# Optimization experiments

Hardware: AMD Instinct MI355X
Metric: run time of the kernel (lower is better)

The kernel has to match this reference:

```python
import jax, jax.numpy as jnp
import numpy as np

B, T, C = 4, 1024, 2048
H, DN, DR = 16, 128, 64
D = DN + DR  # 192
Q_RANK, KV_RANK = 1536, 512
ROPE_BASE = 10000.0


def rope_cos_sin(seq_len, dim, dtype=jnp.float32):
    inv_freq = 1.0 / (ROPE_BASE ** (jnp.arange(0, dim, 2, dtype=jnp.float32) / dim))
    t = jnp.arange(seq_len, dtype=jnp.float32)
    freqs = jnp.outer(t, inv_freq)  # [T, dim/2]
    return jnp.cos(freqs).astype(dtype), jnp.sin(freqs).astype(dtype)


def apply_rope(x, cos, sin):
    # x: [B, T, H, Dr], cos/sin: [T, Dr/2]; interleaved-pair rotation (Llama style)
    x1 = x[..., 0::2]
    x2 = x[..., 1::2]
    c = cos[None, :, None, :]
    s = sin[None, :, None, :]
    o1 = x1 * c - x2 * s
    o2 = x1 * s + x2 * c
    return jnp.stack([o1, o2], axis=-1).reshape(x.shape)


def setup_inputs() -> dict:
    key = jax.random.key(0)
    ks = jax.random.split(key, 9)
    def g(k, shape, scale):
        return jax.random.normal(k, shape, dtype=jnp.float32) * scale
    return {
        "x": g(ks[0], (B, T, C), 1.0),
        "wq_down": g(ks[1], (C, Q_RANK), C ** -0.5),
        "wq_nope": g(ks[2], (Q_RANK, H * DN), Q_RANK ** -0.5),
        "wq_rope": g(ks[3], (Q_RANK, H * DR), Q_RANK ** -0.5),
        "wkv_down": g(ks[4], (C, KV_RANK), C ** -0.5),
        "wv_up": g(ks[5], (KV_RANK, H * D), KV_RANK ** -0.5),
        "wk_nope": g(ks[6], (KV_RANK, H * DN), KV_RANK ** -0.5),
        "wk_rope": g(ks[7], (KV_RANK, H * DR), KV_RANK ** -0.5),
        "wo": g(ks[8], (H * D, C), (H * D) ** -0.5),
    }


def reference(x, wq_down, wq_nope, wq_rope, wkv_down, wv_up, wk_nope, wk_rope, wo):
    b, t, c = x.shape
    q_latent = x @ wq_down            # [B,T,Q_RANK]
    kv_latent = x @ wkv_down          # [B,T,KV_RANK]
    q_c = (q_latent @ wq_nope).reshape(b, t, H, DN)
    q_r = (q_latent @ wq_rope).reshape(b, t, H, DR)
    v = (kv_latent @ wv_up).reshape(b, t, H, D)
    k_c = (kv_latent @ wk_nope).reshape(b, t, H, DN)
    k_r = (kv_latent @ wk_rope).reshape(b, t, H, DR)

    cos, sin = rope_cos_sin(t, DR, x.dtype)
    q_r = apply_rope(q_r, cos, sin)
    k_r = apply_rope(k_r, cos, sin)

    q = jnp.concatenate([q_c, q_r], axis=-1)  # [B,T,H,D]
    k = jnp.concatenate([k_c, k_r], axis=-1)  # [B,T,H,D]

    scale = 1.0 / (D ** 0.5)
    scores = jnp.einsum("bthd,bshd->bhts", q, k) * scale  # [B,H,T,T]
    causal = jnp.tril(jnp.ones((t, t), dtype=bool))
    scores = jnp.where(causal[None, None], scores, jnp.finfo(scores.dtype).min)
    probs = jax.nn.softmax(scores, axis=-1)
    out = jnp.einsum("bhts,bshd->bthd", probs, v).reshape(b, t, H * D)
    return out @ wo
```

## Files before the change

kernel.cpp:

```cpp
#include <hip/hip_runtime.h>

typedef unsigned short u16;
typedef __bf16  bf16x8 __attribute__((ext_vector_type(8)));
typedef short   short8 __attribute__((ext_vector_type(8)));
typedef float   f32x4  __attribute__((ext_vector_type(4)));
typedef u16     u16x4  __attribute__((ext_vector_type(4)));

__device__ __forceinline__ u16 f2bf(float f) {
  unsigned b = __builtin_bit_cast(unsigned, f);
  b += 0x7fffu + ((b >> 16) & 1u);
  return (u16)(b >> 16);
}
__device__ __forceinline__ float bf2f(u16 u) {
  return __builtin_bit_cast(float, (unsigned)u << 16);
}
__device__ __forceinline__ f32x4 mfma16(short8 a, short8 b, f32x4 c) {
  return __builtin_amdgcn_mfma_f32_16x16x32_bf16(
      __builtin_bit_cast(bf16x8, a), __builtin_bit_cast(bf16x8, b), c, 0, 0, 0);
}
__device__ __forceinline__ void gload_lds16(const void* g, void* l) {
  __builtin_amdgcn_global_load_lds(
      (const __attribute__((address_space(1))) void*)g,
      (__attribute__((address_space(3))) void*)l, 16, 0, 0);
}

#define VMCNT(n) asm volatile("s_waitcnt vmcnt(" #n ")" ::: "memory")
#define MEMFENCE asm volatile("" ::: "memory")

__global__ __launch_bounds__(256) void castk(const float* __restrict__ in,
                                             u16* __restrict__ out, int n4) {
  int i = blockIdx.x * 256 + threadIdx.x;
  if (i >= n4) return;
  float4 v = ((const float4*)in)[i];
  u16x4 o;
  o[0] = f2bf(v.x); o[1] = f2bf(v.y); o[2] = f2bf(v.z); o[3] = f2bf(v.w);
  *(u16x4*)&out[i * 4] = o;
}

__global__ __launch_bounds__(256) void wcast(
    const float* __restrict__ wqd, const float* __restrict__ wqn,
    const float* __restrict__ wqr, const float* __restrict__ wkd,
    const float* __restrict__ wvu, const float* __restrict__ wkn,
    const float* __restrict__ wkr, const float* __restrict__ wo,
    u16* __restrict__ W1t, u16* __restrict__ Wqt,
    u16* __restrict__ Wkvt, u16* __restrict__ Wot) {
  __shared__ float tile[64][65];
  const int bid = blockIdx.x;
  const float* W; u16* Wt; int K, N, lid;
  if (bid < 768)       { W = wqd; Wt = W1t;                 K = 2048; N = 1536; lid = bid; }
  else if (bid < 1024) { W = wkd; Wt = W1t + 1536ull * 2048; K = 2048; N = 512;  lid = bid - 768; }
  else if (bid < 1792) { W = wqn; Wt = Wqt;                 K = 1536; N = 2048; lid = bid - 1024; }
  else if (bid < 2176) { W = wqr; Wt = Wqt + 2048ull * 1536; K = 1536; N = 1024; lid = bid - 1792; }
  else if (bid < 2432) { W = wkn; Wt = Wkvt;                K = 512;  N = 2048; lid = bid - 2176; }
  else if (bid < 2560) { W = wkr; Wt = Wkvt + 2048ull * 512; K = 512;  N = 1024; lid = bid - 2432; }
  else if (bid < 2944) { W = wvu; Wt = Wkvt + 3072ull * 512; K = 512;  N = 3072; lid = bid - 2560; }
  else                 { W = wo;  Wt = Wot;                 K = 3072; N = 2048; lid = bid - 2944; }
  const int kb = K >> 6;
  const int k0 = (lid % kb) * 64, n0 = (lid / kb) * 64;
  const int tc = threadIdx.x & 63, tr = threadIdx.x >> 6;
#pragma unroll
  for (int r = tr; r < 64; r += 4)
    tile[r][tc] = W[(size_t)(k0 + r) * N + n0 + tc];
  __syncthreads();
#pragma unroll
  for (int r = tr; r < 64; r += 4)
    Wt[(size_t)(n0 + r) * K + k0 + tc] = f2bf(tile[tc][r]);
}

template <int EPI>
__global__ __launch_bounds__(512, 2) void gemm8(const u16* __restrict__ A, int lda,
                                                const u16* __restrict__ Bt, int ldb,
                                                void* __restrict__ out0,
                                                void* __restrict__ out1,
                                                void* __restrict__ out2, int ldc,
                                                int K) {
  __shared__ char smem[98304];
  const int tid = threadIdx.x;
  const int w = tid >> 6, l = tid & 63;
  const int wr = w >> 2, wc = w & 3;
  const int lr = l & 15, lk8b = (l >> 4) << 4, lg4 = (l >> 4) * 4;

  const int nbx = gridDim.x;
  int id = blockIdx.y * nbx + blockIdx.x;
  int cpx = (nbx * gridDim.y) >> 3;
  int sid = (id & 7) * cpx + (id >> 3);
  const int m0 = (sid % nbx) * 128, n0 = (sid / nbx) * 256;

  const int arow = w * 16 + (l >> 2);
  const int acb = ((l & 3) << 4) ^ ((arow & 3) << 4);
  const u16* ag = A + (size_t)(m0 + arow) * lda + (acb >> 1);
  const int brow = w * 32 + (l >> 2);
  const int bcb = ((l & 3) << 4) ^ ((brow & 3) << 4);
  const u16* bg0 = Bt + (size_t)(n0 + brow) * ldb + (bcb >> 1);
  const u16* bg1 = bg0 + (size_t)16 * ldb;

  const int swzf = (lr & 3) << 4;
  int aoff[4], boff[4];
#pragma unroll
  for (int m = 0; m < 4; ++m)
    aoff[m] = (wr * 64 + m * 16 + lr) * 64 + (lk8b ^ swzf);
#pragma unroll
  for (int n = 0; n < 4; ++n)
    boff[n] = (wc * 64 + n * 16 + lr) * 64 + (lk8b ^ swzf);

  f32x4 acc[4][4] = {};

  auto STAGE = [&](int kt) {
    const int koff = kt << 5;
    char* ab = smem + ((kt & 3) << 13);
    char* bb = smem + 32768 + ((kt & 3) << 14);
    gload_lds16(ag + koff, ab + w * 1024);
    gload_lds16(bg0 + koff, bb + w * 2048);
    gload_lds16(bg1 + koff, bb + w * 2048 + 1024);
  };
  auto COMP = [&](int kt) {
    const char* ab = smem + ((kt & 3) << 13);
    const char* bb = smem + 32768 + ((kt & 3) << 14);
    short8 af[4], bf[4];
#pragma unroll
    for (int m = 0; m < 4; ++m) af[m] = *(const short8*)(ab + aoff[m]);
#pragma unroll
    for (int n = 0; n < 4; ++n) bf[n] = *(const short8*)(bb + boff[n]);
    __builtin_amdgcn_s_setprio(1);
#pragma unroll
    for (int m = 0; m < 4; ++m)
#pragma unroll
      for (int n = 0; n < 4; ++n)
        acc[m][n] = mfma16(af[m], bf[n], acc[m][n]);
    __builtin_amdgcn_s_setprio(0);
  };

  const int NT = K >> 5;
  STAGE(0); STAGE(1); STAGE(2);
  for (int kt = 0; kt < NT - 3; ++kt) {
    STAGE(kt + 3);
    VMCNT(9);
    __builtin_amdgcn_s_barrier();
    MEMFENCE;
    COMP(kt);
    MEMFENCE;
    __builtin_amdgcn_s_barrier();
  }
  VMCNT(6); __builtin_amdgcn_s_barrier(); MEMFENCE;
  COMP(NT - 3);
  MEMFENCE; __builtin_amdgcn_s_barrier();
  VMCNT(3); __builtin_amdgcn_s_barrier(); MEMFENCE;
  COMP(NT - 2);
  MEMFENCE; __builtin_amdgcn_s_barrier();
  VMCNT(0); __builtin_amdgcn_s_barrier(); MEMFENCE;
  COMP(NT - 1);
  MEMFENCE; __builtin_amdgcn_s_barrier();

  if (EPI == 3 && n0 >= 3072) {
    u16* ldt = (u16*)smem;
#pragma unroll
    for (int m = 0; m < 4; ++m)
#pragma unroll
      for (int n = 0; n < 4; ++n)
#pragma unroll
        for (int j = 0; j < 4; ++j)
          ldt[(wc * 64 + n * 16 + lr) * 136 + (wr * 64 + m * 16 + lg4 + j)] =
              f2bf(acc[m][n][j]);
    __syncthreads();
    const int b = m0 >> 10, tloc = m0 & 1023, n0v = n0 - 3072;
#pragma unroll
    for (int i = 0; i < 8; ++i) {
      int lin = i * 512 + tid;
      int col = lin >> 4, t16 = lin & 15;
      int cg = n0v + col;
      int h = (unsigned)cg / 192u, d = cg - h * 192;
      short8 vv = *(const short8*)&ldt[col * 136 + t16 * 8];
      *(short8*)((u16*)out2 + ((size_t)(b * 16 + h) * 192 + d) * 1024 + tloc + t16 * 8) = vv;
    }
    return;
  }
#pragma unroll
  for (int m = 0; m < 4; ++m)
#pragma unroll
    for (int n = 0; n < 4; ++n)
#pragma unroll
      for (int j = 0; j < 4; ++j) {
        int r = m0 + wr * 64 + m * 16 + lg4 + j;
        int c = n0 + wc * 64 + n * 16 + lr;
        float v = acc[m][n][j];
        if (EPI == 0) {
          ((u16*)out0)[(size_t)r * ldc + c] = f2bf(v);
        } else if (EPI == 1 || EPI == 3) {
          if (c < 2048) {
            int cc = (c >> 7) * 192 + (c & 127);
            ((u16*)out0)[(size_t)r * ldc + cc] = f2bf(v);
          } else {
            ((u16*)out1)[(size_t)r * 1024 + (c - 2048)] = f2bf(v);
          }
        } else {
          ((float*)out0)[(size_t)r * ldc + c] = v;
        }
      }
}

__global__ __launch_bounds__(256) void rope_k(const u16* __restrict__ qsrc,
                                              const u16* __restrict__ ksrc,
                                              u16* __restrict__ qdst,
                                              u16* __restrict__ kdst) {
  int idx = blockIdx.x * 256 + threadIdx.x;
  int row = idx >> 9;
  int rem = idx & 511;
  int h = rem >> 5, i = rem & 31;
  int tpos = row & 1023;
  float inv = exp2f(-(float)i * 0.4152410118609203f);
  float f = (float)tpos * inv;
  float s, c;
  sincosf(f, &s, &c);
  size_t si = (size_t)row * 1024 + h * 64 + 2 * i;
  size_t o = (size_t)row * 3072 + h * 192 + 128 + 2 * i;
  {
    float x1 = bf2f(qsrc[si]), x2 = bf2f(qsrc[si + 1]);
    qdst[o]     = f2bf(x1 * c - x2 * s);
    qdst[o + 1] = f2bf(x1 * s + x2 * c);
  }
  {
    float x1 = bf2f(ksrc[si]), x2 = bf2f(ksrc[si + 1]);
    kdst[o]     = f2bf(x1 * c - x2 * s);
    kdst[o + 1] = f2bf(x1 * s + x2 * c);
  }
}

__global__ __launch_bounds__(256, 2) void attn_kernel(const u16* __restrict__ Q,
                                                      const u16* __restrict__ K,
                                                      const u16* __restrict__ Vt,
                                                      u16* __restrict__ O) {
  __shared__ char smem[57344];
  const int t = threadIdx.x, w = t >> 6, l = t & 63;
  const int lr = l & 15, hi = l >> 4;
  const int tt = (blockIdx.x + (blockIdx.y >> 3)) & 7;
  const int qidx = (tt < 4) ? 2 * tt : 15 - 2 * tt;
  const int qb = qidx * 128;
  const int b = blockIdx.y >> 4, h = blockIdx.y & 15;
  const int wq0 = qb + w * 32;
  const size_t rs = 3072;
  const u16* Qg = Q + ((size_t)(b * 1024 + qb)) * rs + h * 192;
  const char* Kg = (const char*)(K + ((size_t)b * 1024) * rs + h * 192);
  const char* Vg = (const char*)(Vt + (size_t)(b * 16 + h) * 192 * 1024);
  u16* Og = O + ((size_t)(b * 1024 + qb)) * rs + h * 192;

  char* psw = smem + 49152 + w * 2048;
  const int kswz = (lr & 7) << 4;
  const int pswz = (lr & 3) << 4;

  short8 qfr[2][6];
#pragma unroll
  for (int qf = 0; qf < 2; ++qf)
#pragma unroll
    for (int dc = 0; dc < 6; ++dc)
      qfr[qf][dc] = *(const short8*)(Qg + (size_t)(w * 32 + qf * 16 + lr) * rs + dc * 32 + hi * 8);

  const char* kptr[3];
#pragma unroll
  for (int i = 0; i < 3; ++i) {
    int lin = (i * 4 + w) * 1024 + l * 16;
    int row = lin / 384;
    int col = lin % 384;
    kptr[i] = Kg + (size_t)row * 6144 + (col ^ ((row & 7) << 4));
  }
  const char* vptr[3];
#pragma unroll
  for (int i = 0; i < 3; ++i) {
    int lin = (i * 4 + w) * 1024 + l * 16;
    int row = lin >> 6;
    int col = lin & 63;
    vptr[i] = Vg + (size_t)row * 2048 + (col ^ ((row & 3) << 4));
  }

  f32x4 o[12][2] = {};
  float m[2] = {-1e30f, -1e30f}, ls[2] = {0.f, 0.f};
  const float scale = 0.07216878364870323f;
  const int nkv = 4 * (qidx + 1);

  auto STAGE = [&](int kt) {
    char* kb = smem + (kt & 1) * 24576;
    char* vb = kb + 12288;
#pragma unroll
    for (int i = 0; i < 3; ++i) {
      gload_lds16(kptr[i] + (size_t)kt * 196608, kb + (i * 4 + w) * 1024);
      gload_lds16(vptr[i] + (size_t)kt * 64,     vb + (i * 4 + w) * 1024);
    }
  };

  STAGE(0);
  for (int kt = 0; kt < nkv; ++kt) {
    if (kt + 1 < nkv) { STAGE(kt + 1); VMCNT(6); }
    else              { VMCNT(0); }
    __builtin_amdgcn_s_barrier();
    MEMFENCE;
    const int kv0 = kt << 5;
    const char* ks = smem + (kt & 1) * 24576;
    const char* vs = ks + 12288;

    if (kv0 <= wq0) {
      f32x4 st[2][2] = {};
#pragma unroll
      for (int dc = 0; dc < 6; ++dc) {
        const int kin = (dc * 64 + hi * 16) ^ kswz;
        short8 ka0 = *(const short8*)(ks + lr * 384 + kin);
        short8 ka1 = *(const short8*)(ks + (16 + lr) * 384 + kin);
        st[0][0] = mfma16(ka0, qfr[0][dc], st[0][0]);
        st[0][1] = mfma16(ka0, qfr[1][dc], st[0][1]);
        st[1][0] = mfma16(ka1, qfr[0][dc], st[1][0]);
        st[1][1] = mfma16(ka1, qfr[1][dc], st[1][1]);
      }

      const bool needmask = (kv0 + 31 > wq0);
      float mt[2];
#pragma unroll
      for (int qf = 0; qf < 2; ++qf) {
        const int q = wq0 + qf * 16 + lr;
        float mx = -1e30f;
#pragma unroll
        for (int kf = 0; kf < 2; ++kf)
#pragma unroll
          for (int j = 0; j < 4; ++j) {
            float s = st[kf][qf][j] * scale;
            if (needmask && (kv0 + kf * 16 + hi * 4 + j > q)) s = -1e30f;
            st[kf][qf][j] = s;
            mx = fmaxf(mx, s);
          }
        mx = fmaxf(mx, __shfl_xor(mx, 16));
        mx = fmaxf(mx, __shfl_xor(mx, 32));
        mt[qf] = mx;
      }
      const bool skip = __all((mt[0] <= m[0] + 8.0f) & (mt[1] <= m[1] + 8.0f));
      if (!skip) {
#pragma unroll
        for (int qf = 0; qf < 2; ++qf) {
          float mn = fmaxf(m[qf], mt[qf]);
          float corr = __expf(m[qf] - mn);
          m[qf] = mn;
          ls[qf] *= corr;
#pragma unroll
          for (int nf = 0; nf < 12; ++nf)
#pragma unroll
            for (int j = 0; j < 4; ++j) o[nf][qf][j] *= corr;
        }
      }
#pragma unroll
      for (int qf = 0; qf < 2; ++qf) {
        float sum = 0.f;
        char* pq = psw + (qf * 16 + lr) * 64;
#pragma unroll
        for (int kf = 0; kf < 2; ++kf)
#pragma unroll
          for (int jp = 0; jp < 2; ++jp) {
            float p0 = __expf(st[kf][qf][2 * jp]     - m[qf]);
            float p1 = __expf(st[kf][qf][2 * jp + 1] - m[qf]);
            sum += p0 + p1;
            unsigned pk = (unsigned)f2bf(p0) | ((unsigned)f2bf(p1) << 16);
            int kb = 2 * (kf * 16 + hi * 4 + 2 * jp);
            *(unsigned*)(pq + (kb ^ pswz)) = pk;
          }
        sum += __shfl_xor(sum, 16);
        sum += __shfl_xor(sum, 32);
        ls[qf] += sum;
      }
      asm volatile("s_waitcnt lgkmcnt(0)" ::: "memory");
      __builtin_amdgcn_sched_barrier(0);

      short8 pb0 = *(const short8*)(psw + lr * 64 + ((hi * 16) ^ pswz));
      short8 pb1 = *(const short8*)(psw + (16 + lr) * 64 + ((hi * 16) ^ pswz));
#pragma unroll
      for (int nf = 0; nf < 12; ++nf) {
        short8 va = *(const short8*)(vs + (nf * 16 + lr) * 64 + ((hi * 16) ^ pswz));
        o[nf][0] = mfma16(va, pb0, o[nf][0]);
        o[nf][1] = mfma16(va, pb1, o[nf][1]);
      }
    }
    MEMFENCE;
    __builtin_amdgcn_s_barrier();
  }

#pragma unroll
  for (int qf = 0; qf < 2; ++qf) {
    float inv = 1.0f / ls[qf];
    char* ob = smem + (w * 32 + qf * 16 + lr) * 384;
#pragma unroll
    for (int nf = 0; nf < 12; ++nf)
#pragma unroll
      for (int j = 0; j < 4; ++j)
        *(u16*)(ob + ((nf * 32 + hi * 8 + 2 * j) ^ kswz)) = f2bf(o[nf][qf][j] * inv);
  }
  __syncthreads();
#pragma unroll
  for (int i = 0; i < 12; ++i) {
    int idx = i * 256 + t;
    int row = idx / 24;
    int c16 = idx % 24;
    short8 vv = *(const short8*)(smem + row * 384 + ((c16 * 16) ^ ((row & 7) << 4)));
    *(short8*)((char*)Og + (size_t)row * 6144 + c16 * 16) = vv;
  }
}

extern "C" void kernel_launch(void* const* d_in, const int* in_sizes, int n_in,
                              void* d_out, int out_size, void* d_ws, size_t ws_size,
                              hipStream_t stream) {
  const float* x   = (const float*)d_in[0];
  const float* wqd = (const float*)d_in[1];
  const float* wqn = (const float*)d_in[2];
  const float* wqr = (const float*)d_in[3];
  const float* wkd = (const float*)d_in[4];
  const float* wvu = (const float*)d_in[5];
  const float* wkn = (const float*)d_in[6];
  const float* wkr = (const float*)d_in[7];
  const float* wo  = (const float*)d_in[8];

  char* ws = (char*)d_ws;
  size_t off = 0;
  auto alloc = [&](size_t bytes) {
    char* p = ws + off;
    off += (bytes + 255) & ~(size_t)255;
    return p;
  };
  u16* xb   = (u16*)alloc(8388608ull * 2);
  u16* W1t  = (u16*)alloc(2048ull * 2048 * 2);
  u16* Wqt  = (u16*)alloc(3072ull * 1536 * 2);
  u16* Wkvt = (u16*)alloc(6144ull * 512 * 2);
  u16* Wot  = (u16*)alloc(2048ull * 3072 * 2);
  u16* lat  = (u16*)alloc(4096ull * 2048 * 2);
  u16* Qb   = (u16*)alloc(4096ull * 3072 * 2);
  u16* Kb   = (u16*)alloc(4096ull * 3072 * 2);
  u16* Vt   = (u16*)alloc(4096ull * 3072 * 2);
  u16* AO   = (u16*)alloc(4096ull * 3072 * 2);
  u16* qrt  = (u16*)alloc(4096ull * 1024 * 2);
  u16* krt  = (u16*)alloc(4096ull * 1024 * 2);

  castk<<<8192, 256, 0, stream>>>(x, xb, 2097152);

  wcast<<<4480, 256, 0, stream>>>(wqd, wqn, wqr, wkd, wvu, wkn, wkr, wo,
                                  W1t, Wqt, Wkvt, Wot);

  gemm8<0><<<dim3(32, 8), 512, 0, stream>>>(xb, 2048, W1t, 2048, lat, nullptr, nullptr, 2048, 2048);
  gemm8<1><<<dim3(32, 12), 512, 0, stream>>>(lat, 2048, Wqt, 1536, Qb, qrt, nullptr, 3072, 1536);
  gemm8<3><<<dim3(32, 24), 512, 0, stream>>>(lat + 1536, 2048, Wkvt, 512, Kb, krt, Vt, 3072, 512);

  rope_k<<<8192, 256, 0, stream>>>(qrt, krt, Qb, Kb);

  attn_kernel<<<dim3(8, 64), 256, 0, stream>>>(Qb, Kb, Vt, AO);

  gemm8<2><<<dim3(32, 8), 512, 0, stream>>>(AO, 3072, Wot, 3072, d_out, nullptr, nullptr, 2048, 3072);
}
```

Before: 320.3 us.

## Rework GEMM mainloop with 64-wide K tiles and triple-buffered split prefetch

Replaces the GEMM mainloop's 32-wide K tiles and 4-stage ring with 64-wide K tiles in a 3-buffer ring (144KB LDS) and an XOR swizzle over 128-byte rows. Each iteration now uses one barrier. The global-to-LDS prefetch for tile kt+2 is split into two parts, issued between two half-K MFMA phases and ordered with explicit lgkmcnt waits and sched barriers. The aim is to cut barrier count and overlap loads with compute. The cost is higher LDS use, which rules out a second resident block, plus an extra __syncthreads before the LDS-reusing epilogue.

Measured after the change: 279.2 us. 12.8% less time.

```diff
diff --git a/kernel.cpp b/kernel.cpp
--- a/kernel.cpp
+++ b/kernel.cpp
@@ -25,6 +25,7 @@
 }
 
 #define VMCNT(n) asm volatile("s_waitcnt vmcnt(" #n ")" ::: "memory")
+#define LGKMCNT(n) asm volatile("s_waitcnt lgkmcnt(" #n ")" ::: "memory")
 #define MEMFENCE asm volatile("" ::: "memory")
 
 __global__ __launch_bounds__(256) void castk(const float* __restrict__ in,
@@ -68,17 +69,17 @@
 }
 
 template <int EPI>
-__global__ __launch_bounds__(512, 2) void gemm8(const u16* __restrict__ A, int lda,
-                                                const u16* __restrict__ Bt, int ldb,
-                                                void* __restrict__ out0,
-                                                void* __restrict__ out1,
-                                                void* __restrict__ out2, int ldc,
-                                                int K) {
-  __shared__ char smem[98304];
+__global__ __launch_bounds__(512, 2) void gemm_p8(const u16* __restrict__ A, int lda,
+                                                  const u16* __restrict__ Bt, int ldb,
+                                                  void* __restrict__ out0,
+                                                  void* __restrict__ out1,
+                                                  void* __restrict__ out2, int ldc,
+                                                  int K) {
+  __shared__ char smem[147456];
   const int tid = threadIdx.x;
   const int w = tid >> 6, l = tid & 63;
   const int wr = w >> 2, wc = w & 3;
-  const int lr = l & 15, lk8b = (l >> 4) << 4, lg4 = (l >> 4) * 4;
+  const int lr = l & 15, hi = l >> 4, lg4 = hi * 4;
 
   const int nbx = gridDim.x;
   int id = blockIdx.y * nbx + blockIdx.x;
@@ -86,72 +87,92 @@
   int sid = (id & 7) * cpx + (id >> 3);
   const int m0 = (sid % nbx) * 128, n0 = (sid / nbx) * 256;
 
-  const int arow = w * 16 + (l >> 2);
-  const int acb = ((l & 3) << 4) ^ ((arow & 3) << 4);
-  const u16* ag = A + (size_t)(m0 + arow) * lda + (acb >> 1);
-  const int brow = w * 32 + (l >> 2);
-  const int bcb = ((l & 3) << 4) ^ ((brow & 3) << 4);
-  const u16* bg0 = Bt + (size_t)(n0 + brow) * ldb + (bcb >> 1);
-  const u16* bg1 = bg0 + (size_t)16 * ldb;
-
-  const int swzf = (lr & 3) << 4;
+  const u16* asrc[2];
+  const u16* bsrc[4];
+#pragma unroll
+  for (int j = 0; j < 2; ++j) {
+    int lin = j * 8192 + tid * 16;
+    int row = lin >> 7, colb = lin & 127;
+    asrc[j] = A + (size_t)(m0 + row) * lda + ((colb ^ ((row & 7) << 4)) >> 1);
+  }
+#pragma unroll
+  for (int j = 0; j < 4; ++j) {
+    int lin = j * 8192 + tid * 16;
+    int row = lin >> 7, colb = lin & 127;
+    bsrc[j] = Bt + (size_t)(n0 + row) * ldb + ((colb ^ ((row & 7) << 4)) >> 1);
+  }
+
   int aoff[4], boff[4];
 #pragma unroll
-  for (int m = 0; m < 4; ++m)
-    aoff[m] = (wr * 64 + m * 16 + lr) * 64 + (lk8b ^ swzf);
-#pragma unroll
-  for (int n = 0; n < 4; ++n)
-    boff[n] = (wc * 64 + n * 16 + lr) * 64 + (lk8b ^ swzf);
+  for (int m = 0; m < 4; ++m) {
+    int row = wr * 64 + m * 16 + lr;
+    aoff[m] = row * 128 + ((hi * 16) ^ ((row & 7) << 4));
+  }
+#pragma unroll
+  for (int n = 0; n < 4; ++n) {
+    int row = wc * 64 + n * 16 + lr;
+    boff[n] = 16384 + row * 128 + ((hi * 16) ^ ((row & 7) << 4));
+  }
+
+  auto STAGE0 = [&](int kt) {
+    char* buf = smem + 49152 * (kt % 3) + (w << 10);
+    const int ke = kt << 6;
+    gload_lds16(asrc[0] + ke, buf);
+    gload_lds16(asrc[1] + ke, buf + 8192);
+    gload_lds16(bsrc[0] + ke, buf + 16384);
+    gload_lds16(bsrc[1] + ke, buf + 24576);
+  };
+  auto STAGE1 = [&](int kt) {
+    char* buf = smem + 49152 * (kt % 3) + (w << 10);
+    const int ke = kt << 6;
+    gload_lds16(bsrc[2] + ke, buf + 32768);
+    gload_lds16(bsrc[3] + ke, buf + 40960);
+  };
 
   f32x4 acc[4][4] = {};
-
-  auto STAGE = [&](int kt) {
-    const int koff = kt << 5;
-    char* ab = smem + ((kt & 3) << 13);
-    char* bb = smem + 32768 + ((kt & 3) << 14);
-    gload_lds16(ag + koff, ab + w * 1024);
-    gload_lds16(bg0 + koff, bb + w * 2048);
-    gload_lds16(bg1 + koff, bb + w * 2048 + 1024);
-  };
-  auto COMP = [&](int kt) {
-    const char* ab = smem + ((kt & 3) << 13);
-    const char* bb = smem + 32768 + ((kt & 3) << 14);
-    short8 af[4], bf[4];
-#pragma unroll
-    for (int m = 0; m < 4; ++m) af[m] = *(const short8*)(ab + aoff[m]);
-#pragma unroll
-    for (int n = 0; n < 4; ++n) bf[n] = *(const short8*)(bb + boff[n]);
-    __builtin_amdgcn_s_setprio(1);
-#pragma unroll
-    for (int m = 0; m < 4; ++m)
-#pragma unroll
-      for (int n = 0; n < 4; ++n)
-        acc[m][n] = mfma16(af[m], bf[n], acc[m][n]);
-    __builtin_amdgcn_s_setprio(0);
-  };
-
-  const int NT = K >> 5;
-  STAGE(0); STAGE(1); STAGE(2);
-  for (int kt = 0; kt < NT - 3; ++kt) {
-    STAGE(kt + 3);
-    VMCNT(9);
+  const int NT = K >> 6;
+
+  STAGE0(0); STAGE1(0); STAGE0(1); STAGE1(1);
+
+  for (int kt = 0; kt < NT; ++kt) {
+    if (kt < NT - 1) { VMCNT(6); } else { VMCNT(0); }
     __builtin_amdgcn_s_barrier();
     MEMFENCE;
-    COMP(kt);
+    const char* buf = smem + 49152 * (kt % 3);
+    short8 a0[4], b0[4], a1[4], b1[4];
+#pragma unroll
+    for (int m = 0; m < 4; ++m) a0[m] = *(const short8*)(buf + aoff[m]);
+#pragma unroll
+    for (int n = 0; n < 4; ++n) b0[n] = *(const short8*)(buf + boff[n]);
+    __builtin_amdgcn_sched_barrier(0);
+#pragma unroll
+    for (int m = 0; m < 4; ++m) a1[m] = *(const short8*)(buf + (aoff[m] ^ 64));
+#pragma unroll
+    for (int n = 0; n < 4; ++n) b1[n] = *(const short8*)(buf + (boff[n] ^ 64));
+    if (kt + 2 < NT) STAGE0(kt + 2);
+    LGKMCNT(8);
+    __builtin_amdgcn_sched_barrier(0);
+    __builtin_amdgcn_s_setprio(1);
+#pragma unroll
+    for (int m = 0; m < 4; ++m)
+#pragma unroll
+      for (int n = 0; n < 4; ++n) acc[m][n] = mfma16(a0[m], b0[n], acc[m][n]);
+    __builtin_amdgcn_s_setprio(0);
+    __builtin_amdgcn_sched_barrier(0);
+    if (kt + 2 < NT) STAGE1(kt + 2);
+    LGKMCNT(0);
+    __builtin_amdgcn_sched_barrier(0);
+    __builtin_amdgcn_s_setprio(1);
+#pragma unroll
+    for (int m = 0; m < 4; ++m)
+#pragma unroll
+      for (int n = 0; n < 4; ++n) acc[m][n] = mfma16(a1[m], b1[n], acc[m][n]);
+    __builtin_amdgcn_s_setprio(0);
     MEMFENCE;
-    __builtin_amdgcn_s_barrier();
-  }
-  VMCNT(6); __builtin_amdgcn_s_barrier(); MEMFENCE;
-  COMP(NT - 3);
-  MEMFENCE; __builtin_amdgcn_s_barrier();
-  VMCNT(3); __builtin_amdgcn_s_barrier(); MEMFENCE;
-  COMP(NT - 2);
-  MEMFENCE; __builtin_amdgcn_s_barrier();
-  VMCNT(0); __builtin_amdgcn_s_barrier(); MEMFENCE;
-  COMP(NT - 1);
-  MEMFENCE; __builtin_amdgcn_s_barrier();
+  }
 
   if (EPI == 3 && n0 >= 3072) {
+    __syncthreads();
     u16* ldt = (u16*)smem;
 #pragma unroll
     for (int m = 0; m < 4; ++m)
@@ -436,13 +457,13 @@
   wcast<<<4480, 256, 0, stream>>>(wqd, wqn, wqr, wkd, wvu, wkn, wkr, wo,
                                   W1t, Wqt, Wkvt, Wot);
 
-  gemm8<0><<<dim3(32, 8), 512, 0, stream>>>(xb, 2048, W1t, 2048, lat, nullptr, nullptr, 2048, 2048);
-  gemm8<1><<<dim3(32, 12), 512, 0, stream>>>(lat, 2048, Wqt, 1536, Qb, qrt, nullptr, 3072, 1536);
-  gemm8<3><<<dim3(32, 24), 512, 0, stream>>>(lat + 1536, 2048, Wkvt, 512, Kb, krt, Vt, 3072, 512);
+  gemm_p8<0><<<dim3(32, 8), 512, 0, stream>>>(xb, 2048, W1t, 2048, lat, nullptr, nullptr, 2048, 2048);
+  gemm_p8<1><<<dim3(32, 12), 512, 0, stream>>>(lat, 2048, Wqt, 1536, Qb, qrt, nullptr, 3072, 1536);
+  gemm_p8<3><<<dim3(32, 24), 512, 0, stream>>>(lat + 1536, 2048, Wkvt, 512, Kb, krt, Vt, 3072, 512);
 
   rope_k<<<8192, 256, 0, stream>>>(qrt, krt, Qb, Kb);
 
   attn_kernel<<<dim3(8, 64), 256, 0, stream>>>(Qb, Kb, Vt, AO);
 
-  gemm8<2><<<dim3(32, 8), 512, 0, stream>>>(AO, 3072, Wot, 3072, d_out, nullptr, nullptr, 2048, 3072);
-}
+  gemm_p8<2><<<dim3(32, 8), 512, 0, stream>>>(AO, 3072, Wot, 3072, d_out, nullptr, nullptr, 2048, 3072);
+}
```
